# Performance work log

Hardware: AMD Instinct MI355X
Metric: run time of the kernel (lower is better)

The kernel has to match this reference:

```python
import jax, jax.numpy as jnp
import numpy as np

WIN_SIZE = 9
SIGMA = 1.5
K1, K2 = 0.01, 0.03
ALPHA, BETA = 0.5, 1.0
DATA_RANGE = 2.0
COV_NORM = 1.0  # use_sample_covariance=False


def _gaussian_window():
    coords = jnp.arange(WIN_SIZE, dtype=jnp.float32) - WIN_SIZE // 2
    g = jnp.exp(-coords ** 2 / (2.0 * SIGMA ** 2))
    g = g / g.sum()
    w2d = jnp.outer(g, g)  # [9, 9]
    return w2d[None, None, :, :]  # [1, 1, 9, 9] (OIHW, in_channel=1)


def setup_inputs() -> dict:
    key = jax.random.key(0)
    k1, k2 = jax.random.split(key)
    shape = (32, 1, 1024, 1024)
    X = jax.random.uniform(k1, shape, dtype=jnp.float32) * 2.0 - 1.0
    Y = jax.random.uniform(k2, shape, dtype=jnp.float32) * 2.0 - 1.0
    w = _gaussian_window()
    return {"X": X, "Y": Y, "w": w}


def _dwconv(x, w):
    # depthwise (groups=1 here since in_channel=1), VALID padding (use_pad=False)
    return jax.lax.conv_general_dilated(
        x, w, window_strides=(1, 1), padding="VALID",
        dimension_numbers=("NCHW", "OIHW", "NCHW"), feature_group_count=1)


def reference(X, Y, w):
    C1 = (K1 * DATA_RANGE) ** 2
    C2 = (K2 * DATA_RANGE) ** 2
    ux = _dwconv(X, w)
    uy = _dwconv(Y, w)
    uxx = _dwconv(X * X, w)
    uyy = _dwconv(Y * Y, w)
    uxy = _dwconv(X * Y, w)
    vx = COV_NORM * (uxx - ux * ux)
    vy = COV_NORM * (uyy - uy * uy)
    vxy = COV_NORM * (uxy - ux * uy)
    A1 = 2.0 * ux * uy + C1
    A2 = 2.0 * vxy + C2
    B1 = ux ** 2 + uy ** 2 + C1
    B2 = vx + vy + C2
    S = (A1 * A2) / (B1 * B2)
    ssim_loss = (1.0 - S).mean()
    loss_l1 = jnp.abs(X - Y).mean()
    return ALPHA * ssim_loss + BETA * loss_l1
```

## Files before the change

kernel.cpp:

```cpp
#include <hip/hip_runtime.h>

#define NT 256
#define RROWS 45
#define STRIP 256
#define PW 264
#define NLD 132
#define WID 1024
#define HEI 1024
#define OWD 1016

typedef float v2f __attribute__((ext_vector_type(2)));

template<int I> struct IC { static constexpr int v = I; };
template<int N, int I = 0, typename F>
__device__ __forceinline__ void sfor(F&& f) {
    if constexpr (I < N) { f(IC<I>{}); sfor<N, I + 1>(f); }
}

static __device__ __forceinline__ v2f pkfma(v2f a, v2f b, v2f c) {
#if __has_builtin(__builtin_elementwise_fma)
    return __builtin_elementwise_fma(a, b, c);
#else
    v2f r; r.x = fmaf(a.x, b.x, c.x); r.y = fmaf(a.y, b.y, c.y); return r;
#endif
}

__global__ __launch_bounds__(NT, 2)
void ssim_main(const float* __restrict__ X, const float* __restrict__ Y,
               const float* __restrict__ Wg, double* __restrict__ acc)
{
    __shared__ float2 Prow[9][PW];
    __shared__ float  wsum[4][2];

    const int t  = threadIdx.x;
    const int r0 = blockIdx.x * RROWS;
    const int c0 = blockIdx.y * STRIP;
    const size_t ibase = (size_t)blockIdx.z * (size_t)(WID * HEI);

    const bool ldv  = (t < NLD) && (c0 + 2 * t < WID);
    const bool ownc = (t < 128);

    float g[9];
    {
        float s = 0.f;
        sfor<9>([&](auto K) { constexpr int k = decltype(K)::v;
            g[k] = Wg[36 + k]; s += g[k]; });
        float rs = __builtin_amdgcn_rcpf(s);
        sfor<9>([&](auto K) { constexpr int k = decltype(K)::v; g[k] *= rs; });
    }

    const float C1 = 0.0004f, C2 = 0.0036f;
    float ssim_acc = 0.f, l1_acc = 0.f;

    v2f  r01[9], r23[9];
    float r4[9];
    float2 pbx[3], pby[3];

    const float2* __restrict__ Xp = (const float2*)(X + ibase + c0);
    const float2* __restrict__ Yp = (const float2*)(Y + ibase + c0);

    auto issue = [&](int ro, auto S) {
        constexpr int s = decltype(S)::v;
        const int row = r0 + ro;
        if (ldv && row < HEI) {
            pbx[s] = Xp[(size_t)row * (WID / 2) + t];
            pby[s] = Yp[(size_t)row * (WID / 2) + t];
        }
    };
    auto store = [&](int ro, auto S, auto LS) {
        constexpr int s  = decltype(S)::v;
        constexpr int ls = decltype(LS)::v;
        const int row = r0 + ro;
        if (ldv && row < HEI) {
            float4* dst = (float4*)&Prow[ls][2 * t];
            *dst = make_float4(pbx[s].x, pby[s].x, pbx[s].y, pby[s].y);
            if (ownc && ro < RROWS)
                l1_acc += fabsf(pbx[s].x - pby[s].x) + fabsf(pbx[s].y - pby[s].y);
        }
    };
    auto hcomp = [&](auto LS, auto RS) {
        constexpr int ls = decltype(LS)::v;
        constexpr int rs = decltype(RS)::v;
        v2f s01 = (v2f)0.f, s23 = (v2f)0.f; float s4 = 0.f;
        sfor<9>([&](auto K) { constexpr int k = decltype(K)::v;
            float2 p = Prow[ls][t + k];
            v2f a = { p.x, p.y };
            v2f gk2 = { g[k], g[k] };
            s01 = pkfma(gk2, a, s01);
            s23 = pkfma(gk2, a * a, s23);
            s4  = fmaf(g[k], p.x * p.y, s4);
        });
        r01[rs] = s01; r23[rs] = s23; r4[rs] = s4;
    };

    const bool vA = (c0 + t < OWD);

    auto outrow = [&](int j, auto JM) {
        constexpr int jm = decltype(JM)::v;
        if (r0 + j < OWD) {
            v2f u01 = (v2f)0.f, u23 = (v2f)0.f; float u4 = 0.f;
            sfor<9>([&](auto K) { constexpr int k = decltype(K)::v;
                constexpr int s = (jm + k) % 9;
                v2f gk2 = { g[k], g[k] };
                u01 = pkfma(gk2, r01[s], u01);
                u23 = pkfma(gk2, r23[s], u23);
                u4  = fmaf(g[k], r4[s], u4);
            });
            float ux = u01.x, uy = u01.y, uxx = u23.x, uyy = u23.y, uxy = u4;
            float uxux = ux * ux, uyuy = uy * uy, uxuy = ux * uy;
            float A1 = 2.f * uxuy + C1;
            float A2 = 2.f * (uxy - uxuy) + C2;
            float B1 = uxux + uyuy + C1;
            float B2 = (uxx - uxux) + (uyy - uyuy) + C2;
            float S  = (A1 * A2) * __builtin_amdgcn_rcpf(B1 * B2);
            ssim_acc += vA ? S : 0.f;
        }
    };

    issue(0, IC<0>{}); issue(1, IC<1>{}); issue(2, IC<2>{});
    store(0, IC<0>{}, IC<0>{}); store(1, IC<1>{}, IC<1>{}); store(2, IC<2>{}, IC<2>{});
    __syncthreads();
    issue(3, IC<0>{}); issue(4, IC<1>{}); issue(5, IC<2>{});
    hcomp(IC<0>{}, IC<0>{}); hcomp(IC<1>{}, IC<1>{}); hcomp(IC<2>{}, IC<2>{});

    store(3, IC<0>{}, IC<3>{}); store(4, IC<1>{}, IC<4>{}); store(5, IC<2>{}, IC<5>{});
    __syncthreads();
    issue(6, IC<0>{}); issue(7, IC<1>{}); issue(8, IC<2>{});
    hcomp(IC<3>{}, IC<3>{}); hcomp(IC<4>{}, IC<4>{}); hcomp(IC<5>{}, IC<5>{});

    store(6, IC<0>{}, IC<6>{}); store(7, IC<1>{}, IC<7>{}); store(8, IC<2>{}, IC<8>{});
    __syncthreads();
    issue(9, IC<0>{}); issue(10, IC<1>{}); issue(11, IC<2>{});
    hcomp(IC<6>{}, IC<6>{}); hcomp(IC<7>{}, IC<7>{});

#pragma unroll 1
    for (int P = 0; P < 5; ++P) {
        const int jb = 9 * P;
        sfor<3>([&](auto Q) {
            constexpr int q = decltype(Q)::v;
            const int p  = 3 * P + q;
            const int j0 = jb + 3 * q;
            store(j0 + 9,  IC<0>{}, IC<(3 * q) % 9>{});
            store(j0 + 10, IC<1>{}, IC<(3 * q + 1) % 9>{});
            store(j0 + 11, IC<2>{}, IC<(3 * q + 2) % 9>{});
            __syncthreads();
            if (p < 14) {
                issue(j0 + 12, IC<0>{}); issue(j0 + 13, IC<1>{}); issue(j0 + 14, IC<2>{});
            }
            hcomp(IC<(3 * q + 8) % 9>{}, IC<(3 * q + 8) % 9>{});
            outrow(j0,     IC<(3 * q) % 9>{});
            hcomp(IC<(3 * q + 9) % 9>{}, IC<(3 * q + 9) % 9>{});
            outrow(j0 + 1, IC<(3 * q + 1) % 9>{});
            hcomp(IC<(3 * q + 10) % 9>{}, IC<(3 * q + 10) % 9>{});
            outrow(j0 + 2, IC<(3 * q + 2) % 9>{});
        });
    }

#pragma unroll
    for (int off = 32; off > 0; off >>= 1) {
        ssim_acc += __shfl_down(ssim_acc, off);
        l1_acc   += __shfl_down(l1_acc, off);
    }
    const int wid = t >> 6;
    if ((t & 63) == 0) { wsum[wid][0] = ssim_acc; wsum[wid][1] = l1_acc; }
    __syncthreads();
    if (t == 0) {
        double s = 0.0, l = 0.0;
#pragma unroll
        for (int w = 0; w < 4; ++w) { s += (double)wsum[w][0]; l += (double)wsum[w][1]; }
        atomicAdd(acc + 0, s);
        atomicAdd(acc + 1, l);
    }
}

__global__ void ssim_final(const double* __restrict__ acc, float* __restrict__ out)
{
    const double n_ssim = 33032192.0;
    const double n_l1   = 33554432.0;
    double ssim_loss = 1.0 - acc[0] / n_ssim;
    double l1        = acc[1] / n_l1;
    out[0] = (float)(0.5 * ssim_loss + 1.0 * l1);
}

extern "C" void kernel_launch(void* const* d_in, const int* in_sizes, int n_in,
                              void* d_out, int out_size, void* d_ws, size_t ws_size,
                              hipStream_t stream)
{
    const float* X  = (const float*)d_in[0];
    const float* Y  = (const float*)d_in[1];
    const float* Wg = (const float*)d_in[2];
    float*  out = (float*)d_out;
    double* acc = (double*)d_ws;

    hipMemsetAsync(acc, 0, 2 * sizeof(double), stream);
    dim3 grid(23, 4, 32);
    ssim_main<<<grid, NT, 0, stream>>>(X, Y, Wg, acc);
    ssim_final<<<1, 1, 0, stream>>>(acc, out);
}
```

Before: 318.6 us.

## Compute two output columns per thread with halved block size and shared row loads

Halves the block to 128 threads, each producing two adjacent output columns. The horizontal pass reads 10 shared-memory values as float4 and reuses them for both columns, and the vertical pass and SSIM combine are done for the pair with one reciprocal per pair. Packed FMA/mul are forced through inline asm, and the 8-column halo is loaded by the first 4 threads. This cuts LDS traffic and per-output instruction count, at the cost of roughly doubled register pressure and lower thread-level parallelism per block.

```diff
diff --git a/kernel.cpp b/kernel.cpp
--- a/kernel.cpp
+++ b/kernel.cpp
@@ -1,10 +1,9 @@
 #include <hip/hip_runtime.h>
 
-#define NT 256
+#define NT 128
 #define RROWS 45
 #define STRIP 256
 #define PW 264
-#define NLD 132
 #define WID 1024
 #define HEI 1024
 #define OWD 1016
@@ -18,43 +17,45 @@
 }
 
 static __device__ __forceinline__ v2f pkfma(v2f a, v2f b, v2f c) {
-#if __has_builtin(__builtin_elementwise_fma)
-    return __builtin_elementwise_fma(a, b, c);
-#else
-    v2f r; r.x = fmaf(a.x, b.x, c.x); r.y = fmaf(a.y, b.y, c.y); return r;
-#endif
+    v2f d;
+    asm("v_pk_fma_f32 %0, %1, %2, %3" : "=v"(d) : "v"(a), "v"(b), "v"(c));
+    return d;
+}
+static __device__ __forceinline__ v2f pkmul(v2f a, v2f b) {
+    v2f d;
+    asm("v_pk_mul_f32 %0, %1, %2" : "=v"(d) : "v"(a), "v"(b));
+    return d;
 }
 
 __global__ __launch_bounds__(NT, 2)
 void ssim_main(const float* __restrict__ X, const float* __restrict__ Y,
                const float* __restrict__ Wg, double* __restrict__ acc)
 {
-    __shared__ float2 Prow[9][PW];
-    __shared__ float  wsum[4][2];
+    __shared__ float4 Prow[9][PW / 2];
+    __shared__ float  wsum[2][2];
 
     const int t  = threadIdx.x;
     const int r0 = blockIdx.x * RROWS;
     const int c0 = blockIdx.y * STRIP;
     const size_t ibase = (size_t)blockIdx.z * (size_t)(WID * HEI);
-
-    const bool ldv  = (t < NLD) && (c0 + 2 * t < WID);
-    const bool ownc = (t < 128);
-
-    float g[9];
+    const bool hcond = (t < 4) && (c0 + STRIP < WID);
+
+    v2f g2[9];
     {
-        float s = 0.f;
+        float gt[9]; float s = 0.f;
         sfor<9>([&](auto K) { constexpr int k = decltype(K)::v;
-            g[k] = Wg[36 + k]; s += g[k]; });
+            gt[k] = Wg[36 + k]; s += gt[k]; });
         float rs = __builtin_amdgcn_rcpf(s);
-        sfor<9>([&](auto K) { constexpr int k = decltype(K)::v; g[k] *= rs; });
+        sfor<9>([&](auto K) { constexpr int k = decltype(K)::v;
+            float gk = gt[k] * rs; g2[k] = (v2f){gk, gk}; });
     }
 
     const float C1 = 0.0004f, C2 = 0.0036f;
     float ssim_acc = 0.f, l1_acc = 0.f;
 
-    v2f  r01[9], r23[9];
-    float r4[9];
-    float2 pbx[3], pby[3];
+    v2f  rA01[9], rA23[9], rB01[9], rB23[9];
+    float rA4[9], rB4[9];
+    float2 px_[3], py_[3], hx_[3], hy_[3];
 
     const float2* __restrict__ Xp = (const float2*)(X + ibase + c0);
     const float2* __restrict__ Yp = (const float2*)(Y + ibase + c0);
@@ -62,58 +63,87 @@
     auto issue = [&](int ro, auto S) {
         constexpr int s = decltype(S)::v;
         const int row = r0 + ro;
-        if (ldv && row < HEI) {
-            pbx[s] = Xp[(size_t)row * (WID / 2) + t];
-            pby[s] = Yp[(size_t)row * (WID / 2) + t];
+        if (row < HEI) {
+            const size_t rb = (size_t)row * (WID / 2);
+            px_[s] = Xp[rb + t];  py_[s] = Yp[rb + t];
+            if (hcond) { hx_[s] = Xp[rb + 128 + t]; hy_[s] = Yp[rb + 128 + t]; }
         }
     };
     auto store = [&](int ro, auto S, auto LS) {
         constexpr int s  = decltype(S)::v;
         constexpr int ls = decltype(LS)::v;
         const int row = r0 + ro;
-        if (ldv && row < HEI) {
-            float4* dst = (float4*)&Prow[ls][2 * t];
-            *dst = make_float4(pbx[s].x, pby[s].x, pbx[s].y, pby[s].y);
-            if (ownc && ro < RROWS)
-                l1_acc += fabsf(pbx[s].x - pby[s].x) + fabsf(pbx[s].y - pby[s].y);
+        if (row < HEI) {
+            Prow[ls][t] = make_float4(px_[s].x, py_[s].x, px_[s].y, py_[s].y);
+            if (hcond) Prow[ls][128 + t] = make_float4(hx_[s].x, hy_[s].x, hx_[s].y, hy_[s].y);
+            if (ro < RROWS)
+                l1_acc += fabsf(px_[s].x - py_[s].x) + fabsf(px_[s].y - py_[s].y);
         }
     };
-    auto hcomp = [&](auto LS, auto RS) {
+
+    auto hcomp2 = [&](auto LS, auto RS) {
         constexpr int ls = decltype(LS)::v;
         constexpr int rs = decltype(RS)::v;
-        v2f s01 = (v2f)0.f, s23 = (v2f)0.f; float s4 = 0.f;
+        const float4* rowp = &Prow[ls][0];
+        v2f a[10];
+        sfor<5>([&](auto I) { constexpr int i = decltype(I)::v;
+            float4 f = rowp[t + i];
+            a[2 * i]     = (v2f){f.x, f.y};
+            a[2 * i + 1] = (v2f){f.z, f.w};
+        });
+        v2f aa[10]; float xy[10];
+        sfor<10>([&](auto E) { constexpr int e = decltype(E)::v;
+            aa[e] = pkmul(a[e], a[e]);
+            xy[e] = a[e].x * a[e].y;
+        });
+        v2f hA01 = (v2f)0.f, hA23 = (v2f)0.f, hB01 = (v2f)0.f, hB23 = (v2f)0.f;
+        float hA4 = 0.f, hB4 = 0.f;
         sfor<9>([&](auto K) { constexpr int k = decltype(K)::v;
-            float2 p = Prow[ls][t + k];
-            v2f a = { p.x, p.y };
-            v2f gk2 = { g[k], g[k] };
-            s01 = pkfma(gk2, a, s01);
-            s23 = pkfma(gk2, a * a, s23);
-            s4  = fmaf(g[k], p.x * p.y, s4);
-        });
-        r01[rs] = s01; r23[rs] = s23; r4[rs] = s4;
-    };
-
-    const bool vA = (c0 + t < OWD);
-
-    auto outrow = [&](int j, auto JM) {
+            hA01 = pkfma(g2[k], a[k],      hA01);
+            hA23 = pkfma(g2[k], aa[k],     hA23);
+            hA4  = fmaf(g2[k].x, xy[k],     hA4);
+            hB01 = pkfma(g2[k], a[k + 1],  hB01);
+            hB23 = pkfma(g2[k], aa[k + 1], hB23);
+            hB4  = fmaf(g2[k].x, xy[k + 1], hB4);
+        });
+        rA01[rs] = hA01; rA23[rs] = hA23; rA4[rs] = hA4;
+        rB01[rs] = hB01; rB23[rs] = hB23; rB4[rs] = hB4;
+    };
+
+    const bool vA = (c0 + 2 * t < OWD);
+    const bool vB = (c0 + 2 * t + 1 < OWD);
+
+    auto outrow2 = [&](int j, auto JM) {
         constexpr int jm = decltype(JM)::v;
         if (r0 + j < OWD) {
-            v2f u01 = (v2f)0.f, u23 = (v2f)0.f; float u4 = 0.f;
+            v2f uA01 = (v2f)0.f, uA23 = (v2f)0.f, uB01 = (v2f)0.f, uB23 = (v2f)0.f;
+            float uA4 = 0.f, uB4 = 0.f;
             sfor<9>([&](auto K) { constexpr int k = decltype(K)::v;
                 constexpr int s = (jm + k) % 9;
-                v2f gk2 = { g[k], g[k] };
-                u01 = pkfma(gk2, r01[s], u01);
-                u23 = pkfma(gk2, r23[s], u23);
-                u4  = fmaf(g[k], r4[s], u4);
+                uA01 = pkfma(g2[k], rA01[s], uA01);
+                uA23 = pkfma(g2[k], rA23[s], uA23);
+                uA4  = fmaf(g2[k].x, rA4[s], uA4);
+                uB01 = pkfma(g2[k], rB01[s], uB01);
+                uB23 = pkfma(g2[k], rB23[s], uB23);
+                uB4  = fmaf(g2[k].x, rB4[s], uB4);
             });
-            float ux = u01.x, uy = u01.y, uxx = u23.x, uyy = u23.y, uxy = u4;
-            float uxux = ux * ux, uyuy = uy * uy, uxuy = ux * uy;
-            float A1 = 2.f * uxuy + C1;
-            float A2 = 2.f * (uxy - uxuy) + C2;
-            float B1 = uxux + uyuy + C1;
-            float B2 = (uxx - uxux) + (uyy - uyuy) + C2;
-            float S  = (A1 * A2) * __builtin_amdgcn_rcpf(B1 * B2);
-            ssim_acc += vA ? S : 0.f;
+            auto nb = [&](v2f u01, v2f u23, float uxy, float& n, float& b) {
+                v2f uu = pkmul(u01, u01);
+                float sq   = uu.x + uu.y;
+                float uxuy = u01.x * u01.y;
+                float A1 = fmaf(2.f, uxuy, C1);
+                float A2 = fmaf(2.f, uxy - uxuy, C2);
+                float B1 = sq + C1;
+                float B2 = (u23.x + u23.y) - sq + C2;
+                n = A1 * A2; b = B1 * B2;
+            };
+            float nA, bA, nB, bB;
+            nb(uA01, uA23, uA4, nA, bA);
+            nb(uB01, uB23, uB4, nB, bB);
+            nA = vA ? nA : 0.f;
+            nB = vB ? nB : 0.f;
+            float num = fmaf(nA, bB, nB * bA);
+            ssim_acc = fmaf(num, __builtin_amdgcn_rcpf(bA * bB), ssim_acc);
         }
     };
 
@@ -121,25 +151,24 @@
     store(0, IC<0>{}, IC<0>{}); store(1, IC<1>{}, IC<1>{}); store(2, IC<2>{}, IC<2>{});
     __syncthreads();
     issue(3, IC<0>{}); issue(4, IC<1>{}); issue(5, IC<2>{});
-    hcomp(IC<0>{}, IC<0>{}); hcomp(IC<1>{}, IC<1>{}); hcomp(IC<2>{}, IC<2>{});
+    hcomp2(IC<0>{}, IC<0>{}); hcomp2(IC<1>{}, IC<1>{}); hcomp2(IC<2>{}, IC<2>{});
 
     store(3, IC<0>{}, IC<3>{}); store(4, IC<1>{}, IC<4>{}); store(5, IC<2>{}, IC<5>{});
     __syncthreads();
     issue(6, IC<0>{}); issue(7, IC<1>{}); issue(8, IC<2>{});
-    hcomp(IC<3>{}, IC<3>{}); hcomp(IC<4>{}, IC<4>{}); hcomp(IC<5>{}, IC<5>{});
+    hcomp2(IC<3>{}, IC<3>{}); hcomp2(IC<4>{}, IC<4>{}); hcomp2(IC<5>{}, IC<5>{});
 
     store(6, IC<0>{}, IC<6>{}); store(7, IC<1>{}, IC<7>{}); store(8, IC<2>{}, IC<8>{});
     __syncthreads();
     issue(9, IC<0>{}); issue(10, IC<1>{}); issue(11, IC<2>{});
-    hcomp(IC<6>{}, IC<6>{}); hcomp(IC<7>{}, IC<7>{});
+    hcomp2(IC<6>{}, IC<6>{}); hcomp2(IC<7>{}, IC<7>{});
 
 #pragma unroll 1
     for (int P = 0; P < 5; ++P) {
-        const int jb = 9 * P;
         sfor<3>([&](auto Q) {
             constexpr int q = decltype(Q)::v;
             const int p  = 3 * P + q;
-            const int j0 = jb + 3 * q;
+            const int j0 = 9 * P + 3 * q;
             store(j0 + 9,  IC<0>{}, IC<(3 * q) % 9>{});
             store(j0 + 10, IC<1>{}, IC<(3 * q + 1) % 9>{});
             store(j0 + 11, IC<2>{}, IC<(3 * q + 2) % 9>{});
@@ -147,12 +176,12 @@
             if (p < 14) {
                 issue(j0 + 12, IC<0>{}); issue(j0 + 13, IC<1>{}); issue(j0 + 14, IC<2>{});
             }
-            hcomp(IC<(3 * q + 8) % 9>{}, IC<(3 * q + 8) % 9>{});
-            outrow(j0,     IC<(3 * q) % 9>{});
-            hcomp(IC<(3 * q + 9) % 9>{}, IC<(3 * q + 9) % 9>{});
-            outrow(j0 + 1, IC<(3 * q + 1) % 9>{});
-            hcomp(IC<(3 * q + 10) % 9>{}, IC<(3 * q + 10) % 9>{});
-            outrow(j0 + 2, IC<(3 * q + 2) % 9>{});
+            hcomp2(IC<(3 * q + 8) % 9>{}, IC<(3 * q + 8) % 9>{});
+            outrow2(j0,     IC<(3 * q) % 9>{});
+            hcomp2(IC<(3 * q + 9) % 9>{}, IC<(3 * q + 9) % 9>{});
+            outrow2(j0 + 1, IC<(3 * q + 1) % 9>{});
+            hcomp2(IC<(3 * q + 10) % 9>{}, IC<(3 * q + 10) % 9>{});
+            outrow2(j0 + 2, IC<(3 * q + 2) % 9>{});
         });
     }
 
@@ -165,9 +194,8 @@
     if ((t & 63) == 0) { wsum[wid][0] = ssim_acc; wsum[wid][1] = l1_acc; }
     __syncthreads();
     if (t == 0) {
-        double s = 0.0, l = 0.0;
-#pragma unroll
-        for (int w = 0; w < 4; ++w) { s += (double)wsum[w][0]; l += (double)wsum[w][1]; }
+        double s = (double)wsum[0][0] + (double)wsum[1][0];
+        double l = (double)wsum[0][1] + (double)wsum[1][1];
         atomicAdd(acc + 0, s);
         atomicAdd(acc + 1, l);
     }
```

Measured after the change: 329.0 us. 1.03x slower.
